# Optimization experiments

Hardware: AMD Instinct MI355X
Metric: run time of the kernel (lower is better)

Reference implementation:

```python
import jax, jax.numpy as jnp
import numpy as np

B, T, C, E, K, CAP, H = 8, 2048, 1024, 8, 2, 4096, 4096


def setup_inputs() -> dict:
    key = jax.random.key(0)
    ks = jax.random.split(key, 6)
    s = 0.02
    return {
        "x": jax.random.normal(ks[0], (B, T, C), jnp.float32),
        "rw1": s * jax.random.normal(ks[1], (C, H), jnp.float32),
        "rb1": jnp.zeros((H,), jnp.float32),
        "rw2": s * jax.random.normal(ks[2], (H, E), jnp.float32),
        "rb2": jnp.zeros((E,), jnp.float32),
        "ew1": s * jax.random.normal(ks[3], (E, C, H), jnp.float32),
        "eb1": jnp.zeros((E, H), jnp.float32),
        "ew2": s * jax.random.normal(ks[4], (E, H, C), jnp.float32),
        "eb2": jnp.zeros((E, C), jnp.float32),
    }


def reference(x, rw1, rb1, rw2, rb2, ew1, eb1, ew2, eb2):
    Bx, Tx, Cx = x.shape
    N = Bx * Tx
    # Router FFN -> gating logits [B,T,E]
    logits = jax.nn.relu(x @ rw1 + rb1) @ rw2 + rb2
    vals, ids = jax.lax.top_k(logits, K)           # [B,T,K]
    probs = jax.nn.softmax(vals, axis=-1)          # [B,T,K]

    ids_f = ids.reshape(N * K)                     # expert id per (token, k) slot
    probs_f = probs.reshape(N * K)
    xr = jnp.repeat(x.reshape(N, Cx), K, axis=0)   # [N*K, C], token order preserved

    # position of each slot within its expert's capacity buffer
    m = jax.nn.one_hot(ids_f, E, dtype=jnp.int32)  # [N*K, E]
    pos = jnp.cumsum(m, axis=0) - 1
    pos_tok = jnp.take_along_axis(pos, ids_f[:, None], axis=1)[:, 0]
    keep = (pos_tok < CAP).astype(x.dtype)         # drop tokens over capacity (padding)
    pos_c = jnp.clip(pos_tok, 0, CAP - 1)

    # dispatch: scatter tokens into per-expert padded buffers [E, CAP, C]
    disp = jnp.zeros((E, CAP, Cx), x.dtype).at[ids_f, pos_c].add(xr * keep[:, None])

    # expert FFN, batched over experts
    h = jax.nn.relu(jnp.einsum('enc,ech->enh', disp, ew1) + eb1[:, None, :])
    eo = jnp.einsum('enh,ehc->enc', h, ew2) + eb2[:, None, :]

    # combine: gather expert outputs back, weight by gate prob, sum over k
    y = eo[ids_f, pos_c] * (probs_f * keep)[:, None]   # [N*K, C]
    return y.reshape(Bx, Tx, K, Cx).sum(axis=2)
```

## Files before the change

kernel.cpp:

```cpp
#include <hip/hip_runtime.h>
#include <cstdint>
#include <type_traits>

#define B_    8
#define T_    2048
#define C_    1024
#define E_    8
#define K_    2
#define CAP_  4096
#define H_    4096
#define NTOK  (B_ * T_)
#define NSLOT (NTOK * K_)
#define KR_   3072

typedef __bf16 bf16x8 __attribute__((ext_vector_type(8)));
typedef float  f32x4  __attribute__((ext_vector_type(4)));

static __device__ __forceinline__ float b2f(unsigned short u) {
    union { float f; unsigned int i; } v; v.i = ((unsigned int)u) << 16; return v.f;
}
static __device__ __forceinline__ unsigned short f2b(float f) {
    unsigned int x = __float_as_uint(f);
    unsigned int r = (x + 0x7fffu + ((x >> 16) & 1u)) >> 16;
    return (unsigned short)r;
}

template<int W> static __device__ __forceinline__ void vm_wait() {
    if constexpr (W == 8) asm volatile("s_waitcnt vmcnt(8)" ::: "memory");
    else if constexpr (W == 4) asm volatile("s_waitcnt vmcnt(4)" ::: "memory");
    else if constexpr (W == 0) asm volatile("s_waitcnt vmcnt(0)" ::: "memory");
}

template<int RELU, typename TC>
__global__ __launch_bounds__(512, 2) void gemm256_pipe(
    const unsigned short* __restrict__ A, const unsigned short* __restrict__ BT,
    const float* __restrict__ bias, TC* __restrict__ Cout,
    int Kd, int Nld, int NT,
    long sA, long sB, long sBias, long sC)
{
    extern __shared__ char smem[];

    const int z = blockIdx.z;
    A    += (size_t)z * sA;
    BT   += (size_t)z * sB;
    bias += (size_t)z * sBias;
    Cout += (size_t)z * sC;

    const int gx = gridDim.x;
    const int nwg = gx * gridDim.y;
    int wg = blockIdx.y * gx + blockIdx.x;
    wg = (wg & 7) * (nwg >> 3) + (wg >> 3);
    const int bm = (wg / gx) * 256;
    const int bn = (wg % gx) * 256;

    const int tid  = threadIdx.x;
    const int lane = tid & 63;
    const int wid  = tid >> 6;
    const int wrow = (wid >> 2) * 128;
    const int wcol = (wid & 3) * 64;
    const int fr = lane & 15;
    const int fq = lane >> 4;

    const size_t rbA = (size_t)Kd * 2;
    const char* Ag = (const char*)A  + (size_t)bm * rbA;
    const char* Bg = (const char*)BT + (size_t)bn * rbA;

    f32x4 acc[8][4];
#pragma unroll
    for (int i = 0; i < 8; i++)
#pragma unroll
        for (int j = 0; j < 4; j++) acc[i][j] = (f32x4){0.f, 0.f, 0.f, 0.f};

    auto STAGE = [&](int t) {
        char* dA = smem + (size_t)(t & 3) * 32768;
        char* dB = dA + 16384;
        const size_t kb = (size_t)t * 64;
#pragma unroll
        for (int r = 0; r < 2; ++r) {
            const int o   = r * 8192 + tid * 16;
            const int row = o >> 6;
            const int sw  = (((o >> 4) & 3) ^ ((row >> 1) & 3)) << 4;
            __builtin_amdgcn_global_load_lds(
                (const __attribute__((address_space(1))) void*)(Ag + (size_t)row * rbA + kb + sw),
                (__attribute__((address_space(3))) void*)(dA + r * 8192 + wid * 1024),
                16, 0, 0);
            __builtin_amdgcn_global_load_lds(
                (const __attribute__((address_space(1))) void*)(Bg + (size_t)row * rbA + kb + sw),
                (__attribute__((address_space(3))) void*)(dB + r * 8192 + wid * 1024),
                16, 0, 0);
        }
    };

    auto COMPUTE = [&](int t) {
        const char* As_ = smem + (size_t)(t & 3) * 32768;
        const char* Bs_ = As_ + 16384;
        bf16x8 a_[8], b_[4];
#pragma unroll
        for (int mi = 0; mi < 8; ++mi) {
            const int row = wrow + mi * 16 + fr;
            a_[mi] = *(const bf16x8*)(As_ + row * 64 + ((fq ^ ((row >> 1) & 3)) << 4));
        }
#pragma unroll
        for (int ni = 0; ni < 4; ++ni) {
            const int row = wcol + ni * 16 + fr;
            b_[ni] = *(const bf16x8*)(Bs_ + row * 64 + ((fq ^ ((row >> 1) & 3)) << 4));
        }
        __builtin_amdgcn_s_barrier();
        asm volatile("s_waitcnt lgkmcnt(0)" ::: "memory");
        __builtin_amdgcn_sched_barrier(0);
        __builtin_amdgcn_s_setprio(1);
#pragma unroll
        for (int mi = 0; mi < 8; ++mi)
#pragma unroll
            for (int ni = 0; ni < 4; ++ni)
                acc[mi][ni] = __builtin_amdgcn_mfma_f32_16x16x32_bf16(
                    a_[mi], b_[ni], acc[mi][ni], 0, 0, 0);
        __builtin_amdgcn_s_setprio(0);
    };

    STAGE(0); STAGE(1); STAGE(2);
    vm_wait<8>();
    __builtin_amdgcn_s_barrier();

    int t = 0;
    for (; t < NT - 3; ++t) {
        STAGE(t + 3);
        COMPUTE(t);
        vm_wait<8>();
        __builtin_amdgcn_s_barrier();
    }
    COMPUTE(NT - 3);
    vm_wait<4>();
    __builtin_amdgcn_s_barrier();
    COMPUTE(NT - 2);
    vm_wait<0>();
    __builtin_amdgcn_s_barrier();
    COMPUTE(NT - 1);

    const float* bias_o = bias;
    asm volatile("" : "+s"(bias_o));
#pragma unroll
    for (int mi = 0; mi < 8; ++mi) {
#pragma unroll
        for (int ni = 0; ni < 4; ++ni) {
            const int c = bn + wcol + ni * 16 + fr;
            const float bv = bias_o[c];
#pragma unroll
            for (int rg = 0; rg < 4; ++rg) {
                const int r = bm + wrow + mi * 16 + fq * 4 + rg;
                float v = acc[mi][ni][rg] + bv;
                if (RELU) v = fmaxf(v, 0.f);
                if constexpr (std::is_same_v<TC, float>)
                    Cout[(size_t)r * Nld + c] = v;
                else
                    Cout[(size_t)r * Nld + c] = f2b(v);
            }
        }
    }
}

__global__ __launch_bounds__(256) void split_x(
    const float* __restrict__ x, unsigned short* __restrict__ A2)
{
    const int n = blockIdx.x;
    const int c = threadIdx.x * 4;
    const float4 v = *(const float4*)(x + (size_t)n * C_ + c);
    ushort4 hi, lo;
    hi.x = f2b(v.x); lo.x = f2b(v.x - b2f(hi.x));
    hi.y = f2b(v.y); lo.y = f2b(v.y - b2f(hi.y));
    hi.z = f2b(v.z); lo.z = f2b(v.z - b2f(hi.z));
    hi.w = f2b(v.w); lo.w = f2b(v.w - b2f(hi.w));
    unsigned short* row = A2 + (size_t)n * KR_;
    *(ushort4*)(row + c)            = hi;
    *(ushort4*)(row + C_ + c)       = lo;
    *(ushort4*)(row + 2 * C_ + c)   = hi;
}

__global__ __launch_bounds__(256) void split_w(
    const float* __restrict__ in, unsigned short* __restrict__ out)
{
    __shared__ float t[32][33];
    const int rb = blockIdx.y * 32;
    const int cb = blockIdx.x * 32;
    const int tr = threadIdx.x >> 3, tc = (threadIdx.x & 7) * 4;
    const float4 v = *(const float4*)(in + (size_t)(rb + tr) * H_ + cb + tc);
    t[tr][tc + 0] = v.x; t[tr][tc + 1] = v.y; t[tr][tc + 2] = v.z; t[tr][tc + 3] = v.w;
    __syncthreads();
    ushort4 hi, lo;
    float f;
    f = t[tc + 0][tr]; hi.x = f2b(f); lo.x = f2b(f - b2f(hi.x));
    f = t[tc + 1][tr]; hi.y = f2b(f); lo.y = f2b(f - b2f(hi.y));
    f = t[tc + 2][tr]; hi.z = f2b(f); lo.z = f2b(f - b2f(hi.z));
    f = t[tc + 3][tr]; hi.w = f2b(f); lo.w = f2b(f - b2f(hi.w));
    unsigned short* row = out + (size_t)(cb + tr) * KR_;
    *(ushort4*)(row + rb + tc)           = hi;
    *(ushort4*)(row + C_ + rb + tc)      = hi;
    *(ushort4*)(row + 2 * C_ + rb + tc)  = lo;
}

__global__ __launch_bounds__(256) void transpose_cvt(
    const float* __restrict__ in, unsigned short* __restrict__ out, int R, int Ncols)
{
    __shared__ float t[32][33];
    const size_t zoff = (size_t)blockIdx.z * R * Ncols;
    in  += zoff;
    out += zoff;
    const int rb = blockIdx.y * 32, cb = blockIdx.x * 32;
    const int tr = threadIdx.x >> 3, tc = (threadIdx.x & 7) * 4;
    const float4 v = *(const float4*)(in + (size_t)(rb + tr) * Ncols + cb + tc);
    t[tr][tc + 0] = v.x; t[tr][tc + 1] = v.y; t[tr][tc + 2] = v.z; t[tr][tc + 3] = v.w;
    __syncthreads();
    ushort4 u;
    u.x = f2b(t[tc + 0][tr]); u.y = f2b(t[tc + 1][tr]);
    u.z = f2b(t[tc + 2][tr]); u.w = f2b(t[tc + 3][tr]);
    *(ushort4*)(out + (size_t)(cb + tr) * R + rb + tc) = u;
}

__global__ __launch_bounds__(256) void router_topk(
    const float* __restrict__ h1, const float* __restrict__ rw2,
    const float* __restrict__ rb2, int* __restrict__ ids, float* __restrict__ probs)
{
    const int n = blockIdx.x;
    const float* hrow = h1 + (size_t)n * H_;
    float acc[E_];
#pragma unroll
    for (int e = 0; e < E_; e++) acc[e] = 0.f;
    for (int h = threadIdx.x; h < H_; h += 256) {
        const float hv = hrow[h];
        const float4 w0 = *(const float4*)(rw2 + (size_t)h * E_);
        const float4 w1 = *(const float4*)(rw2 + (size_t)h * E_ + 4);
        acc[0] = fmaf(hv, w0.x, acc[0]); acc[1] = fmaf(hv, w0.y, acc[1]);
        acc[2] = fmaf(hv, w0.z, acc[2]); acc[3] = fmaf(hv, w0.w, acc[3]);
        acc[4] = fmaf(hv, w1.x, acc[4]); acc[5] = fmaf(hv, w1.y, acc[5]);
        acc[6] = fmaf(hv, w1.z, acc[6]); acc[7] = fmaf(hv, w1.w, acc[7]);
    }
    __shared__ float red[E_][256];
#pragma unroll
    for (int e = 0; e < E_; e++) red[e][threadIdx.x] = acc[e];
    __syncthreads();
    for (int st = 128; st > 0; st >>= 1) {
        if (threadIdx.x < st) {
#pragma unroll
            for (int e = 0; e < E_; e++) red[e][threadIdx.x] += red[e][threadIdx.x + st];
        }
        __syncthreads();
    }
    if (threadIdx.x == 0) {
        float v1 = -1e30f, v2 = -1e30f; int i1 = 0, i2 = 0;
#pragma unroll
        for (int e = 0; e < E_; e++) {
            const float v = red[e][0] + rb2[e];
            if (v > v1)      { v2 = v1; i2 = i1; v1 = v; i1 = e; }
            else if (v > v2) { v2 = v;  i2 = e; }
        }
        const float e2 = expf(v2 - v1);
        const float inv = 1.f / (1.f + e2);
        ids[n * 2] = i1;  ids[n * 2 + 1] = i2;
        probs[n * 2] = inv; probs[n * 2 + 1] = e2 * inv;
    }
}

__global__ __launch_bounds__(256) void compute_pos(
    const int* __restrict__ ids, int* __restrict__ pos)
{
    __shared__ int hist[256][E_];
    const int t = threadIdx.x;
    const int per = NSLOT / 256;
    int cnt[E_];
#pragma unroll
    for (int e = 0; e < E_; e++) cnt[e] = 0;
    const int s0 = t * per;
    for (int i = 0; i < per; i++) cnt[ids[s0 + i]]++;
#pragma unroll
    for (int e = 0; e < E_; e++) hist[t][e] = cnt[e];
    __syncthreads();
    if (t < E_) {
        int run = 0;
        for (int i = 0; i < 256; i++) { const int c = hist[i][t]; hist[i][t] = run; run += c; }
    }
    __syncthreads();
    int run[E_];
#pragma unroll
    for (int e = 0; e < E_; e++) run[e] = hist[t][e];
    for (int i = 0; i < per; i++) { const int e = ids[s0 + i]; pos[s0 + i] = run[e]++; }
}

__global__ __launch_bounds__(256) void dispatch_k(
    const float* __restrict__ x, const int* __restrict__ ids,
    const int* __restrict__ pos, unsigned short* __restrict__ disp)
{
    const int s = blockIdx.x;
    const int e = ids[s], p = pos[s];
    if (p >= CAP_) return;
    const int n = s >> 1;
    const float4 v = *(const float4*)(x + (size_t)n * C_ + threadIdx.x * 4);
    ushort4 u;
    u.x = f2b(v.x); u.y = f2b(v.y); u.z = f2b(v.z); u.w = f2b(v.w);
    *(ushort4*)(disp + ((size_t)e * CAP_ + p) * C_ + threadIdx.x * 4) = u;
}

__global__ __launch_bounds__(256) void combine_k(
    const unsigned short* __restrict__ eo, const int* __restrict__ ids,
    const int* __restrict__ pos, const float* __restrict__ probs,
    float* __restrict__ y)
{
    const int n = blockIdx.x;
    const int c = threadIdx.x * 4;
    float r0 = 0.f, r1 = 0.f, r2 = 0.f, r3 = 0.f;
#pragma unroll
    for (int k = 0; k < K_; k++) {
        const int p = pos[2 * n + k];
        if (p >= CAP_) continue;
        const int e = ids[2 * n + k];
        const float w = probs[2 * n + k];
        const ushort4 u = *(const ushort4*)(eo + ((size_t)e * CAP_ + p) * C_ + c);
        r0 = fmaf(w, b2f(u.x), r0); r1 = fmaf(w, b2f(u.y), r1);
        r2 = fmaf(w, b2f(u.z), r2); r3 = fmaf(w, b2f(u.w), r3);
    }
    *(float4*)(y + (size_t)n * C_ + c) = make_float4(r0, r1, r2, r3);
}

extern "C" void kernel_launch(void* const* d_in, const int* in_sizes, int n_in,
                              void* d_out, int out_size, void* d_ws, size_t ws_size,
                              hipStream_t stream)
{
    const float* x   = (const float*)d_in[0];
    const float* rw1 = (const float*)d_in[1];
    const float* rb1 = (const float*)d_in[2];
    const float* rw2 = (const float*)d_in[3];
    const float* rb2 = (const float*)d_in[4];
    const float* ew1 = (const float*)d_in[5];
    const float* eb1 = (const float*)d_in[6];
    const float* ew2 = (const float*)d_in[7];
    const float* eb2 = (const float*)d_in[8];
    float* y = (float*)d_out;

    char* ws = (char*)d_ws;
    float*          h1    = (float*)ws;
    unsigned short* hexp  = (unsigned short*)ws;
    unsigned short* A2    = (unsigned short*)(ws + 268435456L);
    unsigned short* B2    = (unsigned short*)(ws + 369098752L);
    unsigned short* disp  = (unsigned short*)(ws + 268435456L);
    unsigned short* eo    = (unsigned short*)(ws + 268435456L);
    unsigned short* BTW   = (unsigned short*)(ws + 335544320L);
    int*            ids   = (int*)  (ws + 402653184L);
    float*          probs = (float*)(ws + 402784256L);
    int*            pos   = (int*)  (ws + 402915328L);

    const size_t LDSB = 131072;

    split_x<<<NTOK, 256, 0, stream>>>(x, A2);
    {
        dim3 g(H_ / 32, C_ / 32, 1);
        split_w<<<g, 256, 0, stream>>>(rw1, B2);
    }
    {
        dim3 g(H_ / 256, NTOK / 256, 1);
        gemm256_pipe<1, float><<<g, 512, LDSB, stream>>>(
            A2, B2, rb1, h1, KR_, H_, KR_ / 32, 0, 0, 0, 0);
    }
    router_topk<<<NTOK, 256, 0, stream>>>(h1, rw2, rb2, ids, probs);
    compute_pos<<<1, 256, 0, stream>>>(ids, pos);
    dispatch_k<<<NSLOT, 256, 0, stream>>>(x, ids, pos, disp);
    {
        dim3 g(H_ / 32, C_ / 32, E_);
        transpose_cvt<<<g, 256, 0, stream>>>(ew1, BTW, C_, H_);
    }
    {
        dim3 g(H_ / 256, CAP_ / 256, E_);
        gemm256_pipe<1, unsigned short><<<g, 512, LDSB, stream>>>(
            disp, BTW, eb1, hexp, C_, H_, C_ / 32,
            (long)CAP_ * C_, (long)H_ * C_, (long)H_, (long)CAP_ * H_);
    }
    {
        dim3 g(C_ / 32, H_ / 32, E_);
        transpose_cvt<<<g, 256, 0, stream>>>(ew2, BTW, H_, C_);
    }
    {
        dim3 g(C_ / 256, CAP_ / 256, E_);
        gemm256_pipe<0, unsigned short><<<g, 512, LDSB, stream>>>(
            hexp, BTW, eb2, eo, H_, C_, H_ / 32,
            (long)CAP_ * H_, (long)C_ * H_, (long)C_, (long)CAP_ * C_);
    }
    combine_k<<<NTOK, 256, 0, stream>>>(eo, ids, pos, probs, y);
}
```

Measured before the change: 1.313 ms.

## Restructure GEMM main loop into eight-phase ping-pong schedule with 64-wide K tiles

Result: faster. 1.202 ms (-8.4%).

```diff
diff --git a/kernel.cpp b/kernel.cpp
--- a/kernel.cpp
+++ b/kernel.cpp
@@ -16,6 +16,9 @@
 typedef __bf16 bf16x8 __attribute__((ext_vector_type(8)));
 typedef float  f32x4  __attribute__((ext_vector_type(4)));
 
+#define AS1 __attribute__((address_space(1)))
+#define AS3 __attribute__((address_space(3)))
+
 static __device__ __forceinline__ float b2f(unsigned short u) {
     union { float f; unsigned int i; } v; v.i = ((unsigned int)u) << 16; return v.f;
 }
@@ -26,13 +29,12 @@
 }
 
 template<int W> static __device__ __forceinline__ void vm_wait() {
-    if constexpr (W == 8) asm volatile("s_waitcnt vmcnt(8)" ::: "memory");
-    else if constexpr (W == 4) asm volatile("s_waitcnt vmcnt(4)" ::: "memory");
+    if constexpr (W == 4) asm volatile("s_waitcnt vmcnt(4)" ::: "memory");
     else if constexpr (W == 0) asm volatile("s_waitcnt vmcnt(0)" ::: "memory");
 }
 
 template<int RELU, typename TC>
-__global__ __launch_bounds__(512, 2) void gemm256_pipe(
+__global__ __launch_bounds__(512, 2) void gemm256_8ph(
     const unsigned short* __restrict__ A, const unsigned short* __restrict__ BT,
     const float* __restrict__ bias, TC* __restrict__ Cout,
     int Kd, int Nld, int NT,
@@ -71,71 +73,113 @@
 #pragma unroll
         for (int j = 0; j < 4; j++) acc[i][j] = (f32x4){0.f, 0.f, 0.f, 0.f};
 
-    auto STAGE = [&](int t) {
-        char* dA = smem + (size_t)(t & 3) * 32768;
-        char* dB = dA + 16384;
-        const size_t kb = (size_t)t * 64;
-#pragma unroll
-        for (int r = 0; r < 2; ++r) {
-            const int o   = r * 8192 + tid * 16;
-            const int row = o >> 6;
-            const int sw  = (((o >> 4) & 3) ^ ((row >> 1) & 3)) << 4;
+    auto STAGE_A = [&](int kt) {
+        char* d = smem + (size_t)(kt & 1) * 65536;
+        const size_t kb = (size_t)kt * 128;
+#pragma unroll
+        for (int r = 0; r < 4; ++r) {
+            const int o    = r * 8192 + tid * 16;
+            const int row  = o >> 7;
+            const int slot = (o >> 4) & 7;
+            const int ss   = (slot ^ (row & 7)) << 4;
             __builtin_amdgcn_global_load_lds(
-                (const __attribute__((address_space(1))) void*)(Ag + (size_t)row * rbA + kb + sw),
-                (__attribute__((address_space(3))) void*)(dA + r * 8192 + wid * 1024),
-                16, 0, 0);
+                (const AS1 void*)(Ag + (size_t)row * rbA + kb + ss),
+                (AS3 void*)(d + r * 8192 + wid * 1024), 16, 0, 0);
+        }
+    };
+    auto STAGE_B = [&](int kt) {
+        char* d = smem + (size_t)(kt & 1) * 65536 + 32768;
+        const size_t kb = (size_t)kt * 128;
+#pragma unroll
+        for (int r = 0; r < 4; ++r) {
+            const int o    = r * 8192 + tid * 16;
+            const int row  = o >> 7;
+            const int slot = (o >> 4) & 7;
+            const int ss   = (slot ^ (row & 7)) << 4;
             __builtin_amdgcn_global_load_lds(
-                (const __attribute__((address_space(1))) void*)(Bg + (size_t)row * rbA + kb + sw),
-                (__attribute__((address_space(3))) void*)(dB + r * 8192 + wid * 1024),
-                16, 0, 0);
+                (const AS1 void*)(Bg + (size_t)row * rbA + kb + ss),
+                (AS3 void*)(d + r * 8192 + wid * 1024), 16, 0, 0);
         }
     };
 
-    auto COMPUTE = [&](int t) {
-        const char* As_ = smem + (size_t)(t & 3) * 32768;
-        const char* Bs_ = As_ + 16384;
-        bf16x8 a_[8], b_[4];
-#pragma unroll
-        for (int mi = 0; mi < 8; ++mi) {
-            const int row = wrow + mi * 16 + fr;
-            a_[mi] = *(const bf16x8*)(As_ + row * 64 + ((fq ^ ((row >> 1) & 3)) << 4));
-        }
-#pragma unroll
-        for (int ni = 0; ni < 4; ++ni) {
-            const int row = wcol + ni * 16 + fr;
-            b_[ni] = *(const bf16x8*)(Bs_ + row * 64 + ((fq ^ ((row >> 1) & 3)) << 4));
-        }
-        __builtin_amdgcn_s_barrier();
-        asm volatile("s_waitcnt lgkmcnt(0)" ::: "memory");
-        __builtin_amdgcn_sched_barrier(0);
+    auto LDA = [&](int kt, int mi, int kk) -> bf16x8 {
+        const char* base = smem + (size_t)(kt & 1) * 65536;
+        const int row  = wrow + mi * 16 + fr;
+        const int slot = (kk * 4 + fq) ^ (row & 7);
+        return *(const bf16x8*)(base + row * 128 + slot * 16);
+    };
+    auto LDB = [&](int kt, int ni, int kk) -> bf16x8 {
+        const char* base = smem + (size_t)(kt & 1) * 65536 + 32768;
+        const int row  = wcol + ni * 16 + fr;
+        const int slot = (kk * 4 + fq) ^ (row & 7);
+        return *(const bf16x8*)(base + row * 128 + slot * 16);
+    };
+
+    STAGE_A(0); STAGE_B(0); STAGE_B(1);
+    vm_wait<4>();
+    __builtin_amdgcn_s_barrier();
+
+    bf16x8 a[4], bb[4];
+    for (int kt = 0; kt < NT; ++kt) {
+#pragma unroll
+        for (int i = 0; i < 4; ++i) a[i]  = LDA(kt, i, 0);
+#pragma unroll
+        for (int i = 0; i < 4; ++i) bb[i] = LDB(kt, i, 0);
+        if (kt + 1 < NT) STAGE_A(kt + 1);
+        __builtin_amdgcn_s_barrier();
         __builtin_amdgcn_s_setprio(1);
 #pragma unroll
-        for (int mi = 0; mi < 8; ++mi)
+        for (int mi = 0; mi < 4; ++mi)
 #pragma unroll
             for (int ni = 0; ni < 4; ++ni)
                 acc[mi][ni] = __builtin_amdgcn_mfma_f32_16x16x32_bf16(
-                    a_[mi], b_[ni], acc[mi][ni], 0, 0, 0);
+                    a[mi], bb[ni], acc[mi][ni], 0, 0, 0);
         __builtin_amdgcn_s_setprio(0);
-    };
-
-    STAGE(0); STAGE(1); STAGE(2);
-    vm_wait<8>();
-    __builtin_amdgcn_s_barrier();
-
-    int t = 0;
-    for (; t < NT - 3; ++t) {
-        STAGE(t + 3);
-        COMPUTE(t);
-        vm_wait<8>();
-        __builtin_amdgcn_s_barrier();
-    }
-    COMPUTE(NT - 3);
-    vm_wait<4>();
-    __builtin_amdgcn_s_barrier();
-    COMPUTE(NT - 2);
-    vm_wait<0>();
-    __builtin_amdgcn_s_barrier();
-    COMPUTE(NT - 1);
+        __builtin_amdgcn_s_barrier();
+#pragma unroll
+        for (int i = 0; i < 4; ++i) a[i] = LDA(kt, 4 + i, 0);
+        __builtin_amdgcn_s_barrier();
+        __builtin_amdgcn_s_setprio(1);
+#pragma unroll
+        for (int mi = 0; mi < 4; ++mi)
+#pragma unroll
+            for (int ni = 0; ni < 4; ++ni)
+                acc[4 + mi][ni] = __builtin_amdgcn_mfma_f32_16x16x32_bf16(
+                    a[mi], bb[ni], acc[4 + mi][ni], 0, 0, 0);
+        __builtin_amdgcn_s_setprio(0);
+        __builtin_amdgcn_s_barrier();
+#pragma unroll
+        for (int i = 0; i < 4; ++i) a[i]  = LDA(kt, i, 1);
+#pragma unroll
+        for (int i = 0; i < 4; ++i) bb[i] = LDB(kt, i, 1);
+        __builtin_amdgcn_s_barrier();
+        __builtin_amdgcn_s_setprio(1);
+#pragma unroll
+        for (int mi = 0; mi < 4; ++mi)
+#pragma unroll
+            for (int ni = 0; ni < 4; ++ni)
+                acc[mi][ni] = __builtin_amdgcn_mfma_f32_16x16x32_bf16(
+                    a[mi], bb[ni], acc[mi][ni], 0, 0, 0);
+        __builtin_amdgcn_s_setprio(0);
+        __builtin_amdgcn_s_barrier();
+#pragma unroll
+        for (int i = 0; i < 4; ++i) a[i] = LDA(kt, 4 + i, 1);
+        if (kt + 2 < NT) STAGE_B(kt + 2);
+        if (kt + 1 < NT) {
+            if (kt + 2 < NT) vm_wait<4>();
+            else             vm_wait<0>();
+        }
+        __builtin_amdgcn_s_barrier();
+        __builtin_amdgcn_s_setprio(1);
+#pragma unroll
+        for (int mi = 0; mi < 4; ++mi)
+#pragma unroll
+            for (int ni = 0; ni < 4; ++ni)
+                acc[4 + mi][ni] = __builtin_amdgcn_mfma_f32_16x16x32_bf16(
+                    a[mi], bb[ni], acc[4 + mi][ni], 0, 0, 0);
+        __builtin_amdgcn_s_setprio(0);
+        __builtin_amdgcn_s_barrier();
+    }
 
     const float* bias_o = bias;
     asm volatile("" : "+s"(bias_o));
@@ -356,8 +400,8 @@
     }
     {
         dim3 g(H_ / 256, NTOK / 256, 1);
-        gemm256_pipe<1, float><<<g, 512, LDSB, stream>>>(
-            A2, B2, rb1, h1, KR_, H_, KR_ / 32, 0, 0, 0, 0);
+        gemm256_8ph<1, float><<<g, 512, LDSB, stream>>>(
+            A2, B2, rb1, h1, KR_, H_, KR_ / 64, 0, 0, 0, 0);
     }
     router_topk<<<NTOK, 256, 0, stream>>>(h1, rw2, rb2, ids, probs);
     compute_pos<<<1, 256, 0, stream>>>(ids, pos);
@@ -368,8 +412,8 @@
     }
     {
         dim3 g(H_ / 256, CAP_ / 256, E_);
-        gemm256_pipe<1, unsigned short><<<g, 512, LDSB, stream>>>(
-            disp, BTW, eb1, hexp, C_, H_, C_ / 32,
+        gemm256_8ph<1, unsigned short><<<g, 512, LDSB, stream>>>(
+            disp, BTW, eb1, hexp, C_, H_, C_ / 64,
             (long)CAP_ * C_, (long)H_ * C_, (long)H_, (long)CAP_ * H_);
     }
     {
@@ -378,8 +422,8 @@
     }
     {
         dim3 g(C_ / 256, CAP_ / 256, E_);
-        gemm256_pipe<0, unsigned short><<<g, 512, LDSB, stream>>>(
-            hexp, BTW, eb2, eo, H_, C_, H_ / 32,
+        gemm256_8ph<0, unsigned short><<<g, 512, LDSB, stream>>>(
+            hexp, BTW, eb2, eo, H_, C_, H_ / 64,
             (long)CAP_ * H_, (long)C_ * H_, (long)C_, (long)CAP_ * C_);
     }
     combine_k<<<NTOK, 256, 0, stream>>>(eo, ids, pos, probs, y);
```
